# Kernel optimization log

Hardware: AMD Instinct MI355X
Metric: run time of the kernel (lower is better)

## Reference

```python
import jax, jax.numpy as jnp
import numpy as np

H = 8  # num_heads in nn.MultiheadAttention


def setup_inputs() -> dict:
    key = jax.random.key(0)
    ks = jax.random.split(key, 8)
    B, S, D, M = 32, 64, 512, 8192
    query = jax.random.normal(ks[0], (B, S, D), dtype=jnp.float32)
    memory = jax.random.normal(ks[1], (B, S, D), dtype=jnp.float32)
    memory_bank = jax.random.normal(ks[2], (M, D), dtype=jnp.float32)
    # nn.MultiheadAttention params: packed in_proj (3D, D) + bias, out_proj (D, D) + bias
    in_proj_w = jax.random.normal(ks[3], (3 * D, D), dtype=jnp.float32) / np.sqrt(D)
    in_proj_b = jnp.zeros((3 * D,), dtype=jnp.float32)
    out_proj_w = jax.random.normal(ks[4], (D, D), dtype=jnp.float32) / np.sqrt(D)
    out_proj_b = jnp.zeros((D,), dtype=jnp.float32)
    return {
        "query": query,
        "memory": memory,
        "memory_bank": memory_bank,
        "in_proj_w": in_proj_w,
        "in_proj_b": in_proj_b,
        "out_proj_w": out_proj_w,
        "out_proj_b": out_proj_b,
        "ptr": 17,
    }


def _retrieve(query, memory_bank, in_proj_w, in_proj_b, out_proj_w, out_proj_b):
    B, S, D = query.shape
    M = memory_bank.shape[0]
    hd = D // H
    Wq, Wk, Wv = in_proj_w[:D], in_proj_w[D:2 * D], in_proj_w[2 * D:]
    bq, bk, bv = in_proj_b[:D], in_proj_b[D:2 * D], in_proj_b[2 * D:]
    # key/value come from memory_bank expanded over batch -> identical per batch,
    # so project once: [M, D]
    q = (query @ Wq.T + bq).reshape(B, S, H, hd)
    k = (memory_bank @ Wk.T + bk).reshape(M, H, hd)
    v = (memory_bank @ Wv.T + bv).reshape(M, H, hd)
    scale = 1.0 / np.sqrt(hd).astype(np.float32)
    scores = jnp.einsum('bshd,mhd->bhsm', q * scale, k)  # [B,H,S,M]
    attn = jax.nn.softmax(scores, axis=-1)
    out = jnp.einsum('bhsm,mhd->bshd', attn, v).reshape(B, S, D)
    return out @ out_proj_w.T + out_proj_b


def _store(memory, memory_bank, ptr):
    M, D = memory_bank.shape
    flat = memory.reshape(-1, D)  # [N, D], N < M so indices are unique
    N = flat.shape[0]
    idx = (ptr + jnp.arange(N)) % M  # vectorized circular-buffer scatter
    new_bank = memory_bank.at[idx].set(flat)
    new_ptr = (ptr + N) % M
    return new_bank, new_ptr


def reference(query, memory, memory_bank, in_proj_w, in_proj_b, out_proj_w, out_proj_b, ptr):
    retrieved = _retrieve(query, memory_bank, in_proj_w, in_proj_b, out_proj_w, out_proj_b)
    new_bank, _ = _store(memory, memory_bank, ptr)
    return retrieved, new_bank
```

## Files before the change

### kernel.cpp

```cpp
#include <hip/hip_runtime.h>


#define Dm  512
#define Mb  8192
#define BSr 2048

#define QSCALE 0.18033688011112042f

typedef float f32x4 __attribute__((ext_vector_type(4)));
typedef short bf16x4 __attribute__((ext_vector_type(4)));
typedef short bf16x8 __attribute__((ext_vector_type(8)));
typedef unsigned short u16x4 __attribute__((ext_vector_type(4)));
typedef unsigned short u16x8 __attribute__((ext_vector_type(8)));
typedef unsigned u32x4 __attribute__((ext_vector_type(4)));

#define MFMA(a, b, c) __builtin_amdgcn_mfma_f32_16x16x32_bf16((a), (b), (c), 0, 0, 0)

#if __has_builtin(__builtin_amdgcn_exp2f)
#define EXP2F(x) __builtin_amdgcn_exp2f(x)
#else
#define EXP2F(x) __expf((x)*0.6931471805599453f)
#endif

__device__ __forceinline__ unsigned short f32_bf16(float f) {
  unsigned u = __builtin_bit_cast(unsigned, f);
  u += 0x7FFFu + ((u >> 16) & 1u);
  return (unsigned short)(u >> 16);
}
__device__ __forceinline__ float bf16_f32(unsigned short h) {
  unsigned u = ((unsigned)h) << 16;
  return __builtin_bit_cast(float, u);
}
__device__ __forceinline__ unsigned pack_bf16_trunc(float a, float b) {
  return (__builtin_bit_cast(unsigned, a) >> 16) |
         (__builtin_bit_cast(unsigned, b) & 0xFFFF0000u);
}

__device__ __forceinline__ void gload16(const unsigned short* g, unsigned short* l) {
  __builtin_amdgcn_global_load_lds(
      (const __attribute__((address_space(1))) void*)g,
      (__attribute__((address_space(3))) void*)l, 16, 0, 0);
}

__global__ __launch_bounds__(256) void convert_all(
    const float* __restrict__ q, const float* __restrict__ bank,
    const float* __restrict__ Win, const float* __restrict__ bin,
    const float* __restrict__ Wout, const float* __restrict__ bout,
    unsigned short* __restrict__ q_c, unsigned short* __restrict__ bank_c,
    unsigned short* __restrict__ Win_c, unsigned short* __restrict__ bin_c,
    unsigned short* __restrict__ Wout_c, unsigned short* __restrict__ bout_c) {
  const int e = (blockIdx.x * 256 + threadIdx.x) * 4;
  const float* src; unsigned short* dst; int off; int sw;
  if (e < 1048576)      { src = q;    dst = q_c;    off = e;           sw = 1; }
  else if (e < 5242880) { src = bank; dst = bank_c; off = e - 1048576; sw = 1; }
  else if (e < 6029312) { src = Win;  dst = Win_c;  off = e - 5242880; sw = 1; }
  else if (e < 6030848) { src = bin;  dst = bin_c;  off = e - 6029312; sw = 0; }
  else if (e < 6292992) { src = Wout; dst = Wout_c; off = e - 6030848; sw = 1; }
  else                  { src = bout; dst = bout_c; off = e - 6292992; sw = 0; }
  f32x4 v = *(const f32x4*)(src + off);
  u16x4 o;
#pragma unroll
  for (int j = 0; j < 4; ++j) o[j] = f32_bf16(v[j]);
  int doff = off;
  if (sw) {
    const int row = off >> 9, col = off & 511;
    doff = (off & ~511) | ((((col >> 3) ^ (row & 7)) << 3) | (col & 7));
  }
  *(u16x4*)(dst + doff) = o;
}

__global__ __launch_bounds__(256, 2) void proj_fused(
    const unsigned short* __restrict__ q_c,
    const unsigned short* __restrict__ bank_c,
    const unsigned short* __restrict__ Win_c,
    const unsigned short* __restrict__ bin_c,
    unsigned short* __restrict__ q_s,
    unsigned short* __restrict__ k_s,
    unsigned short* __restrict__ vT_s) {
  __shared__ __align__(16) unsigned short sh[32768];
  const int lane = threadIdx.x & 63;
  const int wv   = threadIdx.x >> 6;
  const int l15  = lane & 15;
  const int qd   = lane >> 4;
  const int mh   = wv & 1;
  const int nh   = wv >> 1;

  const unsigned short *Ag, *B0, *B1;
  int h = 0, mbase, nbase = 0;
  const bool iskv = blockIdx.x < 512;
  if (iskv) {
    const int idx = blockIdx.x;
    h     = (idx >> 3) & 7;
    mbase = ((idx & 7) * 8 + (idx >> 6)) * 128;
    Ag = bank_c + mbase * Dm;
    B0 = Win_c + (Dm + h * 64) * Dm;
    B1 = Win_c + (2 * Dm + h * 64) * Dm;
  } else {
    const int idx = blockIdx.x - 512;
    mbase = (idx >> 2) * 128;
    nbase = (idx & 3) * 128;
    Ag = q_c + mbase * Dm;
    B0 = Win_c + nbase * Dm;
    B1 = Win_c + (nbase + 64) * Dm;
  }

  auto Ab = [&](int buf) { return sh + buf * 8192; };
  auto Bb = [&](int buf) { return sh + 16384 + buf * 8192; };

  auto stage = [&](int buf, int t) {
#pragma unroll
    for (int i = 0; i < 4; ++i) {
      const int chunk = i * 256 + wv * 64 + lane;
      const int row = chunk >> 3, c8 = chunk & 7;
      gload16(Ag + row * Dm + (t * 8 + c8) * 8,
              Ab(buf) + (i * 256 + wv * 64) * 8);
    }
#pragma unroll
    for (int i = 0; i < 4; ++i) {
      const int chunk = i * 256 + wv * 64 + lane;
      const int row = chunk >> 3, c8 = chunk & 7;
      const unsigned short* wb = (row < 64) ? B0 + row * Dm : B1 + (row - 64) * Dm;
      gload16(wb + (t * 8 + c8) * 8,
              Bb(buf) + (i * 256 + wv * 64) * 8);
    }
  };

  const f32x4 z4 = {0.f, 0.f, 0.f, 0.f};
  f32x4 acc[4][4];
#pragma unroll
  for (int mt = 0; mt < 4; ++mt)
#pragma unroll
    for (int nt = 0; nt < 4; ++nt) acc[mt][nt] = z4;

  auto compute = [&](int buf) {
#pragma unroll
    for (int ks = 0; ks < 2; ++ks) {
      bf16x8 af[4], bfr[4];
#pragma unroll
      for (int mt = 0; mt < 4; ++mt) {
        const int row = mh * 64 + mt * 16 + l15;
        af[mt] = *(const bf16x8*)(Ab(buf) + row * 64 + (((ks * 4 + qd) ^ (row & 7)) * 8));
      }
#pragma unroll
      for (int nt = 0; nt < 4; ++nt) {
        const int row = nh * 64 + nt * 16 + l15;
        bfr[nt] = *(const bf16x8*)(Bb(buf) + row * 64 + (((ks * 4 + qd) ^ (row & 7)) * 8));
      }
#pragma unroll
      for (int mt = 0; mt < 4; ++mt)
#pragma unroll
        for (int nt = 0; nt < 4; ++nt)
          acc[mt][nt] = MFMA(af[mt], bfr[nt], acc[mt][nt]);
    }
  };

  stage(0, 0);
  __asm__ volatile("s_waitcnt vmcnt(0)" ::: "memory");
  __syncthreads();
#pragma unroll 1
  for (int t = 0; t < 7; ++t) {
    stage((t + 1) & 1, t + 1);
    compute(t & 1);
    __asm__ volatile("s_waitcnt vmcnt(0)" ::: "memory");
    __syncthreads();
  }
  compute(1);
  __syncthreads();

  if (iskv) {
    unsigned short* Kst = sh;
    unsigned short* Vst = sh + 16384;
    if (nh == 0) {
#pragma unroll
      for (int nt = 0; nt < 4; ++nt) {
        const int d = nt * 16 + l15;
        const float bk = bf16_f32(bin_c[Dm + h * 64 + d]);
#pragma unroll
        for (int mt = 0; mt < 4; ++mt)
#pragma unroll
          for (int r = 0; r < 4; ++r) {
            const int m = mh * 64 + mt * 16 + qd * 4 + r;
            Kst[m * 72 + d] = f32_bf16(acc[mt][nt][r] + bk);
          }
      }
    } else {
#pragma unroll
      for (int nt = 0; nt < 4; ++nt) {
        const int d = nt * 16 + l15;
        const float bv = bf16_f32(bin_c[2 * Dm + h * 64 + d]);
#pragma unroll
        for (int mt = 0; mt < 4; ++mt)
#pragma unroll
          for (int r = 0; r < 4; ++r) {
            const int m = mh * 64 + mt * 16 + qd * 4 + r;
            Vst[d * 136 + m] = f32_bf16(acc[mt][nt][r] + bv);
          }
      }
    }
    __syncthreads();
#pragma unroll
    for (int p = 0; p < 4; ++p) {
      const int m  = p * 32 + (threadIdx.x >> 3);
      const int c8 = threadIdx.x & 7;
      *(u16x8*)(k_s + h * (Mb * 64) + (mbase + m) * 64 + ((c8 ^ (m & 7)) * 8)) =
          *(const u16x8*)(Kst + m * 72 + c8 * 8);
    }
#pragma unroll
    for (int p = 0; p < 4; ++p) {
      const int d    = p * 16 + (threadIdx.x >> 4);
      const int m16  = threadIdx.x & 15;
      const int base = (m16 >> 2) * 32;
      const int q4   = (m16 & 3) * 4;
      u16x4 lo = *(const u16x4*)(Vst + d * 136 + base + q4);
      u16x4 hi = *(const u16x4*)(Vst + d * 136 + base + 16 + q4);
      u16x8 o  = __builtin_shufflevector(lo, hi, 0, 1, 2, 3, 4, 5, 6, 7);
      *(u16x8*)(vT_s + (h * 64 + d) * Mb + mbase + ((m16 ^ (d & 7)) * 8)) = o;
    }
  } else {
#pragma unroll
    for (int nt = 0; nt < 4; ++nt) {
      const int n = nbase + nh * 64 + nt * 16 + l15;
      const float bf = bf16_f32(bin_c[n]);
#pragma unroll
      for (int mt = 0; mt < 4; ++mt)
#pragma unroll
        for (int r = 0; r < 4; ++r) {
          const int m = mbase + mh * 64 + mt * 16 + qd * 4 + r;
          const unsigned idx = ((unsigned)(m >> 6) * 8u + (unsigned)(n >> 6)) * 4096u +
                               (unsigned)(m & 63) * 64u + (unsigned)(n & 63);
          q_s[idx] = f32_bf16((acc[mt][nt][r] + bf) * QSCALE);
        }
    }
  }
}

__global__ __launch_bounds__(256, 2) void attn_partial(
    const unsigned short* __restrict__ q_s,
    const unsigned short* __restrict__ k_s,
    const unsigned short* __restrict__ vT_s,
    unsigned short* __restrict__ O_part,
    float* __restrict__ l_part) {
  __shared__ __align__(16) unsigned short Kbuf[2][128 * 64];
  __shared__ __align__(16) unsigned short Vbuf[2][64 * 128];

  const int lane = threadIdx.x & 63;
  const int wv   = threadIdx.x >> 6;
  const int l15  = lane & 15;
  const int qd   = lane >> 4;
  const int h    = blockIdx.x & 7;
  const int g    = blockIdx.x >> 3;
  const int part = g & 3;
  const int b    = (g >> 2) * 2 + (wv >> 1);
  const int bh   = b * 8 + h;
  const int s0   = (wv & 1) * 32;

  const unsigned short* kp = k_s  + h * (Mb * 64);
  const unsigned short* vp = vT_s + h * (Mb * 64);
  const int m0p = part * 2048;

  bf16x8 bQ[2][2];
  {
    const unsigned short* qp = q_s + bh * 4096;
#pragma unroll
    for (int sj = 0; sj < 2; ++sj)
#pragma unroll
      for (int ks = 0; ks < 2; ++ks)
        bQ[sj][ks] = *(const bf16x8*)(qp + (s0 + sj * 16 + l15) * 64 + ks * 32 + qd * 8);
  }

  const f32x4 z4 = {0.f, 0.f, 0.f, 0.f};
  f32x4 oacc[2][4];
  float lsum[2] = {0.f, 0.f};
#pragma unroll
  for (int sj = 0; sj < 2; ++sj)
#pragma unroll
    for (int dt = 0; dt < 4; ++dt) oacc[sj][dt] = z4;

  const int swz = (l15 & 7) * 8;

  auto stage = [&](int buf, int m0) {
    const unsigned short* gk = kp + (m0 + wv * 32 + (lane >> 3)) * 64 + (lane & 7) * 8;
    unsigned short* lk = &Kbuf[buf][(wv * 32) * 64];
#pragma unroll
    for (int i = 0; i < 4; ++i) gload16(gk + i * 8 * 64, lk + i * 8 * 64);
    const unsigned short* gv = vp + (wv * 16 + (lane >> 4)) * Mb + m0 + (lane & 15) * 8;
    unsigned short* lv = &Vbuf[buf][(wv * 16) * 128];
#pragma unroll
    for (int i = 0; i < 4; ++i) gload16(gv + i * 4 * Mb, lv + i * 4 * 128);
  };

  auto compute = [&](int buf) {
    const unsigned short* Kb = Kbuf[buf];
    const unsigned short* Vb = Vbuf[buf];
#pragma unroll
    for (int c2 = 0; c2 < 2; ++c2) {
      f32x4 sfr[4][2];
#pragma unroll
      for (int kt = 0; kt < 4; ++kt)
#pragma unroll
        for (int sj = 0; sj < 2; ++sj) sfr[kt][sj] = z4;
#pragma unroll
      for (int kt = 0; kt < 4; ++kt) {
        const int row = c2 * 64 + kt * 16 + l15;
#pragma unroll
        for (int ks = 0; ks < 2; ++ks) {
          bf16x8 aK = *(const bf16x8*)(Kb + row * 64 + ((ks * 32 + qd * 8) ^ swz));
#pragma unroll
          for (int sj = 0; sj < 2; ++sj)
            sfr[kt][sj] = MFMA(aK, bQ[sj][ks], sfr[kt][sj]);
        }
      }
      bf16x8 aP[2][2];
#pragma unroll
      for (int sj = 0; sj < 2; ++sj) {
#pragma unroll
        for (int c = 0; c < 2; ++c) {
          const f32x4 lo = sfr[c * 2][sj];
          const f32x4 hi = sfr[c * 2 + 1][sj];
          float e0 = EXP2F(lo[0]), e1 = EXP2F(lo[1]);
          float e2 = EXP2F(lo[2]), e3 = EXP2F(lo[3]);
          float e4 = EXP2F(hi[0]), e5 = EXP2F(hi[1]);
          float e6 = EXP2F(hi[2]), e7 = EXP2F(hi[3]);
          lsum[sj] += ((e0 + e1) + (e2 + e3)) + ((e4 + e5) + (e6 + e7));
          u32x4 pk;
          pk[0] = pack_bf16_trunc(e0, e1);
          pk[1] = pack_bf16_trunc(e2, e3);
          pk[2] = pack_bf16_trunc(e4, e5);
          pk[3] = pack_bf16_trunc(e6, e7);
          aP[sj][c] = __builtin_bit_cast(bf16x8, pk);
        }
      }
#pragma unroll
      for (int c = 0; c < 2; ++c) {
#pragma unroll
        for (int dt = 0; dt < 4; ++dt) {
          const int d = dt * 16 + l15;
          bf16x8 bV = *(const bf16x8*)(Vb + d * 128 + ((c2 * 64 + c * 32 + qd * 8) ^ swz));
#pragma unroll
          for (int sj = 0; sj < 2; ++sj)
            oacc[sj][dt] = MFMA(aP[sj][c], bV, oacc[sj][dt]);
        }
      }
    }
  };

  stage(0, m0p);
  __asm__ volatile("s_waitcnt vmcnt(0)" ::: "memory");
  __syncthreads();
#pragma unroll 1
  for (int t = 0; t < 15; ++t) {
    stage((t + 1) & 1, m0p + (t + 1) * 128);
    compute(t & 1);
    __asm__ volatile("s_waitcnt vmcnt(0)" ::: "memory");
    __syncthreads();
  }
  compute(1);

#pragma unroll
  for (int sj = 0; sj < 2; ++sj) {
    float v = lsum[sj];
    v += __shfl_xor(v, 16);
    v += __shfl_xor(v, 32);
    if (qd == 0) l_part[(bh * 4 + part) * 64 + s0 + sj * 16 + l15] = v;
  }

  unsigned short* Ob = O_part + (bh * 4 + part) * 4096;
#pragma unroll
  for (int sj = 0; sj < 2; ++sj)
#pragma unroll
    for (int dt = 0; dt < 4; ++dt)
#pragma unroll
      for (int r = 0; r < 4; ++r)
        Ob[(s0 + sj * 16 + qd * 4 + r) * 64 + dt * 16 + l15] = f32_bf16(oacc[sj][dt][r]);
}

__global__ __launch_bounds__(256) void combine_bank(
    const unsigned short* __restrict__ O_part, const float* __restrict__ l_part,
    unsigned short* __restrict__ a_stage,
    const float* __restrict__ memory, const float* __restrict__ bank,
    const int* __restrict__ ptrp, float* __restrict__ out_bank) {
  if (blockIdx.x < 1024) {
    const int e  = (blockIdx.x * 256 + threadIdx.x) * 4;
    const int bh = e >> 12;
    const int rem = e & 4095;
    const int s  = rem >> 6;
    const int d  = rem & 63;
    float acc[4] = {0.f, 0.f, 0.f, 0.f};
    float l = 0.f;
#pragma unroll
    for (int p = 0; p < 4; ++p) {
      u16x4 v = *(const u16x4*)(O_part + (bh * 4 + p) * 4096 + rem);
#pragma unroll
      for (int j = 0; j < 4; ++j) acc[j] += bf16_f32(v[j]);
      l += l_part[(bh * 4 + p) * 64 + s];
    }
    const int b = bh >> 3, h = bh & 7;
    u16x4 o;
#pragma unroll
    for (int j = 0; j < 4; ++j) o[j] = f32_bf16(acc[j] / l);
    const int row = b * 64 + s;
    const int col = h * 64 + d;
    const int scol = (((col >> 3) ^ (row & 7)) << 3) | (col & 7);
    *(u16x4*)(a_stage + row * 512 + scol) = o;
  } else {
    const int t  = (blockIdx.x - 1024) * 256 + threadIdx.x;
    const int r  = t >> 7;
    const int c4 = (t & 127) * 4;
    const int ptr = ptrp[0];
    const unsigned off = (unsigned)(r - ptr + Mb) & (Mb - 1);
    const float* src = (off < (unsigned)BSr) ? memory + off * Dm + c4
                                             : bank + r * Dm + c4;
    *(f32x4*)(out_bank + r * Dm + c4) = *(const f32x4*)src;
  }
}

__global__ __launch_bounds__(256, 2) void out_proj(
    const unsigned short* __restrict__ A,
    const unsigned short* __restrict__ W,
    const unsigned short* __restrict__ bias,
    float* __restrict__ out) {
  __shared__ __align__(16) unsigned short sh[32768];
  const int lane = threadIdx.x & 63;
  const int wv   = threadIdx.x >> 6;
  const int l15  = lane & 15;
  const int qd   = lane >> 4;
  const int mh   = wv & 1;
  const int nh   = wv >> 1;

  const int mbase = (blockIdx.x >> 2) * 128;
  const int nbase = (blockIdx.x & 3) * 128;
  const unsigned short* Ag = A + mbase * Dm;
  const unsigned short* B0 = W + nbase * Dm;
  const unsigned short* B1 = W + (nbase + 64) * Dm;

  auto Ab = [&](int buf) { return sh + buf * 8192; };
  auto Bb = [&](int buf) { return sh + 16384 + buf * 8192; };

  auto stage = [&](int buf, int t) {
#pragma unroll
    for (int i = 0; i < 4; ++i) {
      const int chunk = i * 256 + wv * 64 + lane;
      const int row = chunk >> 3, c8 = chunk & 7;
      gload16(Ag + row * Dm + (t * 8 + c8) * 8,
              Ab(buf) + (i * 256 + wv * 64) * 8);
    }
#pragma unroll
    for (int i = 0; i < 4; ++i) {
      const int chunk = i * 256 + wv * 64 + lane;
      const int row = chunk >> 3, c8 = chunk & 7;
      const unsigned short* wb = (row < 64) ? B0 + row * Dm : B1 + (row - 64) * Dm;
      gload16(wb + (t * 8 + c8) * 8,
              Bb(buf) + (i * 256 + wv * 64) * 8);
    }
  };

  const f32x4 z4 = {0.f, 0.f, 0.f, 0.f};
  f32x4 acc[4][4];
#pragma unroll
  for (int mt = 0; mt < 4; ++mt)
#pragma unroll
    for (int nt = 0; nt < 4; ++nt) acc[mt][nt] = z4;

  auto compute = [&](int buf) {
#pragma unroll
    for (int ks = 0; ks < 2; ++ks) {
      bf16x8 af[4], bfr[4];
#pragma unroll
      for (int mt = 0; mt < 4; ++mt) {
        const int row = mh * 64 + mt * 16 + l15;
        af[mt] = *(const bf16x8*)(Ab(buf) + row * 64 + (((ks * 4 + qd) ^ (row & 7)) * 8));
      }
#pragma unroll
      for (int nt = 0; nt < 4; ++nt) {
        const int row = nh * 64 + nt * 16 + l15;
        bfr[nt] = *(const bf16x8*)(Bb(buf) + row * 64 + (((ks * 4 + qd) ^ (row & 7)) * 8));
      }
#pragma unroll
      for (int mt = 0; mt < 4; ++mt)
#pragma unroll
        for (int nt = 0; nt < 4; ++nt)
          acc[mt][nt] = MFMA(af[mt], bfr[nt], acc[mt][nt]);
    }
  };

  stage(0, 0);
  __asm__ volatile("s_waitcnt vmcnt(0)" ::: "memory");
  __syncthreads();
#pragma unroll 1
  for (int t = 0; t < 7; ++t) {
    stage((t + 1) & 1, t + 1);
    compute(t & 1);
    __asm__ volatile("s_waitcnt vmcnt(0)" ::: "memory");
    __syncthreads();
  }
  compute(1);

#pragma unroll
  for (int nt = 0; nt < 4; ++nt) {
    const int n = nbase + nh * 64 + nt * 16 + l15;
    const float bf = bf16_f32(bias[n]);
#pragma unroll
    for (int mt = 0; mt < 4; ++mt)
#pragma unroll
      for (int r = 0; r < 4; ++r) {
        const int m = mbase + mh * 64 + mt * 16 + qd * 4 + r;
        out[m * Dm + n] = acc[mt][nt][r] + bf;
      }
  }
}

extern "C" void kernel_launch(void* const* d_in, const int* in_sizes, int n_in,
                              void* d_out, int out_size, void* d_ws, size_t ws_size,
                              hipStream_t stream) {
  const float* query = (const float*)d_in[0];
  const float* memry = (const float*)d_in[1];
  const float* bank  = (const float*)d_in[2];
  const float* Win   = (const float*)d_in[3];
  const float* bin   = (const float*)d_in[4];
  const float* Wout  = (const float*)d_in[5];
  const float* bout  = (const float*)d_in[6];
  const int*   ptrp  = (const int*)d_in[7];
  float* outf = (float*)d_out;

  char* ws = (char*)d_ws;
  unsigned short* q_c     = (unsigned short*)(ws);
  unsigned short* a_stage = (unsigned short*)(ws);
  unsigned short* bank_c  = (unsigned short*)(ws + (2u << 20));
  unsigned short* O_part  = (unsigned short*)(ws + (2u << 20));
  unsigned short* Win_c   = (unsigned short*)(ws + (10u << 20));
  unsigned short* Wout_c  = (unsigned short*)(ws + 12058624u);
  unsigned short* q_s     = (unsigned short*)(ws + (12u << 20));
  float*          l_part  = (float*)(ws + (14u << 20));
  unsigned short* bin_c   = (unsigned short*)(ws + 14942208u);
  unsigned short* bout_c  = (unsigned short*)(ws + 14945280u);

  unsigned short* kv = (unsigned short*)(outf + 1048576);
  unsigned short* k_s  = kv;
  unsigned short* vT_s = kv + 4194304;

  convert_all<<<6146, 256, 0, stream>>>(query, bank, Win, bin, Wout, bout,
                                        q_c, bank_c, Win_c, bin_c, Wout_c, bout_c);

  proj_fused<<<576, 256, 0, stream>>>(q_c, bank_c, Win_c, bin_c, q_s, k_s, vT_s);

  attn_partial<<<512, 256, 0, stream>>>(q_s, k_s, vT_s, O_part, l_part);

  combine_bank<<<5120, 256, 0, stream>>>(O_part, l_part, a_stage,
                                         memry, bank, ptrp, outf + 1048576);

  out_proj<<<64, 256, 0, stream>>>(a_stage, Wout_c, bout_c, outf);
}
```

Baseline: 160.0 us.

## Split attention key tiles across wave pairs with LDS reduction of partial outputs

```diff
diff --git a/kernel.cpp b/kernel.cpp
--- a/kernel.cpp
+++ b/kernel.cpp
@@ -234,14 +234,14 @@
   }
 }
 
-__global__ __launch_bounds__(256, 2) void attn_partial(
+__global__ __launch_bounds__(512, 4) void attn_partial(
     const unsigned short* __restrict__ q_s,
     const unsigned short* __restrict__ k_s,
     const unsigned short* __restrict__ vT_s,
     unsigned short* __restrict__ O_part,
     float* __restrict__ l_part) {
-  __shared__ __align__(16) unsigned short Kbuf[2][128 * 64];
-  __shared__ __align__(16) unsigned short Vbuf[2][64 * 128];
+  __shared__ __align__(16) unsigned short shmem[2][2][64 * 64];
+  __shared__ float lred[256];
 
   const int lane = threadIdx.x & 63;
   const int wv   = threadIdx.x >> 6;
@@ -250,9 +250,11 @@
   const int h    = blockIdx.x & 7;
   const int g    = blockIdx.x >> 3;
   const int part = g & 3;
-  const int b    = (g >> 2) * 2 + (wv >> 1);
-  const int bh   = b * 8 + h;
-  const int s0   = (wv & 1) * 32;
+  const int bp   = g >> 2;
+  const int bsel = wv >> 2;
+  const int sh_  = (wv >> 1) & 1;
+  const int kh   = (wv & 1) * 32;
+  const int bh   = (bp * 2 + bsel) * 8 + h;
 
   const unsigned short* kp = k_s  + h * (Mb * 64);
   const unsigned short* vp = vT_s + h * (Mb * 64);
@@ -265,7 +267,8 @@
     for (int sj = 0; sj < 2; ++sj)
 #pragma unroll
       for (int ks = 0; ks < 2; ++ks)
-        bQ[sj][ks] = *(const bf16x8*)(qp + (s0 + sj * 16 + l15) * 64 + ks * 32 + qd * 8);
+        bQ[sj][ks] = *(const bf16x8*)(qp + (sh_ * 32 + sj * 16 + l15) * 64 +
+                                      ks * 32 + qd * 8);
   }
 
   const f32x4 z4 = {0.f, 0.f, 0.f, 0.f};
@@ -279,68 +282,51 @@
   const int swz = (l15 & 7) * 8;
 
   auto stage = [&](int buf, int m0) {
-    const unsigned short* gk = kp + (m0 + wv * 32 + (lane >> 3)) * 64 + (lane & 7) * 8;
-    unsigned short* lk = &Kbuf[buf][(wv * 32) * 64];
-#pragma unroll
-    for (int i = 0; i < 4; ++i) gload16(gk + i * 8 * 64, lk + i * 8 * 64);
-    const unsigned short* gv = vp + (wv * 16 + (lane >> 4)) * Mb + m0 + (lane & 15) * 8;
-    unsigned short* lv = &Vbuf[buf][(wv * 16) * 128];
-#pragma unroll
-    for (int i = 0; i < 4; ++i) gload16(gv + i * 4 * Mb, lv + i * 4 * 128);
+    const int r8 = lane >> 3, c8 = lane & 7;
+    gload16(kp + (m0 + wv * 8 + r8) * 64 + c8 * 8, &shmem[buf][0][(wv * 8) * 64]);
+    gload16(vp + (wv * 8 + r8) * Mb + m0 + c8 * 8, &shmem[buf][1][(wv * 8) * 64]);
   };
 
   auto compute = [&](int buf) {
-    const unsigned short* Kb = Kbuf[buf];
-    const unsigned short* Vb = Vbuf[buf];
-#pragma unroll
-    for (int c2 = 0; c2 < 2; ++c2) {
-      f32x4 sfr[4][2];
-#pragma unroll
-      for (int kt = 0; kt < 4; ++kt)
-#pragma unroll
-        for (int sj = 0; sj < 2; ++sj) sfr[kt][sj] = z4;
-#pragma unroll
-      for (int kt = 0; kt < 4; ++kt) {
-        const int row = c2 * 64 + kt * 16 + l15;
-#pragma unroll
-        for (int ks = 0; ks < 2; ++ks) {
-          bf16x8 aK = *(const bf16x8*)(Kb + row * 64 + ((ks * 32 + qd * 8) ^ swz));
-#pragma unroll
-          for (int sj = 0; sj < 2; ++sj)
-            sfr[kt][sj] = MFMA(aK, bQ[sj][ks], sfr[kt][sj]);
-        }
-      }
-      bf16x8 aP[2][2];
-#pragma unroll
-      for (int sj = 0; sj < 2; ++sj) {
-#pragma unroll
-        for (int c = 0; c < 2; ++c) {
-          const f32x4 lo = sfr[c * 2][sj];
-          const f32x4 hi = sfr[c * 2 + 1][sj];
-          float e0 = EXP2F(lo[0]), e1 = EXP2F(lo[1]);
-          float e2 = EXP2F(lo[2]), e3 = EXP2F(lo[3]);
-          float e4 = EXP2F(hi[0]), e5 = EXP2F(hi[1]);
-          float e6 = EXP2F(hi[2]), e7 = EXP2F(hi[3]);
-          lsum[sj] += ((e0 + e1) + (e2 + e3)) + ((e4 + e5) + (e6 + e7));
-          u32x4 pk;
-          pk[0] = pack_bf16_trunc(e0, e1);
-          pk[1] = pack_bf16_trunc(e2, e3);
-          pk[2] = pack_bf16_trunc(e4, e5);
-          pk[3] = pack_bf16_trunc(e6, e7);
-          aP[sj][c] = __builtin_bit_cast(bf16x8, pk);
-        }
-      }
-#pragma unroll
-      for (int c = 0; c < 2; ++c) {
-#pragma unroll
-        for (int dt = 0; dt < 4; ++dt) {
-          const int d = dt * 16 + l15;
-          bf16x8 bV = *(const bf16x8*)(Vb + d * 128 + ((c2 * 64 + c * 32 + qd * 8) ^ swz));
-#pragma unroll
-          for (int sj = 0; sj < 2; ++sj)
-            oacc[sj][dt] = MFMA(aP[sj][c], bV, oacc[sj][dt]);
-        }
-      }
+    const unsigned short* Kb = &shmem[buf][0][0];
+    const unsigned short* Vb = &shmem[buf][1][0];
+    f32x4 sfr[2][2];
+#pragma unroll
+    for (int kt = 0; kt < 2; ++kt)
+#pragma unroll
+      for (int sj = 0; sj < 2; ++sj) sfr[kt][sj] = z4;
+#pragma unroll
+    for (int kt = 0; kt < 2; ++kt) {
+      const int row = kh + kt * 16 + l15;
+#pragma unroll
+      for (int ks = 0; ks < 2; ++ks) {
+        bf16x8 aK = *(const bf16x8*)(Kb + row * 64 + ((ks * 32 + qd * 8) ^ swz));
+#pragma unroll
+        for (int sj = 0; sj < 2; ++sj)
+          sfr[kt][sj] = MFMA(aK, bQ[sj][ks], sfr[kt][sj]);
+      }
+    }
+    bf16x8 aP[2];
+#pragma unroll
+    for (int sj = 0; sj < 2; ++sj) {
+      float e0 = EXP2F(sfr[0][sj][0]), e1 = EXP2F(sfr[0][sj][1]);
+      float e2 = EXP2F(sfr[0][sj][2]), e3 = EXP2F(sfr[0][sj][3]);
+      float e4 = EXP2F(sfr[1][sj][0]), e5 = EXP2F(sfr[1][sj][1]);
+      float e6 = EXP2F(sfr[1][sj][2]), e7 = EXP2F(sfr[1][sj][3]);
+      lsum[sj] += ((e0 + e1) + (e2 + e3)) + ((e4 + e5) + (e6 + e7));
+      u32x4 pk;
+      pk[0] = pack_bf16_trunc(e0, e1);
+      pk[1] = pack_bf16_trunc(e2, e3);
+      pk[2] = pack_bf16_trunc(e4, e5);
+      pk[3] = pack_bf16_trunc(e6, e7);
+      aP[sj] = __builtin_bit_cast(bf16x8, pk);
+    }
+#pragma unroll
+    for (int dt = 0; dt < 4; ++dt) {
+      bf16x8 bV = *(const bf16x8*)(Vb + (dt * 16 + l15) * 64 + ((kh + qd * 8) ^ swz));
+#pragma unroll
+      for (int sj = 0; sj < 2; ++sj)
+        oacc[sj][dt] = MFMA(aP[sj], bV, oacc[sj][dt]);
     }
   };
 
@@ -348,8 +334,8 @@
   __asm__ volatile("s_waitcnt vmcnt(0)" ::: "memory");
   __syncthreads();
 #pragma unroll 1
-  for (int t = 0; t < 15; ++t) {
-    stage((t + 1) & 1, m0p + (t + 1) * 128);
+  for (int t = 0; t < 31; ++t) {
+    stage((t + 1) & 1, m0p + (t + 1) * 64);
     compute(t & 1);
     __asm__ volatile("s_waitcnt vmcnt(0)" ::: "memory");
     __syncthreads();
@@ -361,17 +347,49 @@
     float v = lsum[sj];
     v += __shfl_xor(v, 16);
     v += __shfl_xor(v, 32);
-    if (qd == 0) l_part[(bh * 4 + part) * 64 + s0 + sj * 16 + l15] = v;
-  }
-
-  unsigned short* Ob = O_part + (bh * 4 + part) * 4096;
-#pragma unroll
-  for (int sj = 0; sj < 2; ++sj)
-#pragma unroll
-    for (int dt = 0; dt < 4; ++dt)
-#pragma unroll
-      for (int r = 0; r < 4; ++r)
-        Ob[(s0 + sj * 16 + qd * 4 + r) * 64 + dt * 16 + l15] = f32_bf16(oacc[sj][dt][r]);
+    if (qd == 0) lred[wv * 32 + sj * 16 + l15] = v;
+  }
+  __syncthreads();
+
+  if (threadIdx.x < 128) {
+    const int bs = threadIdx.x >> 6, s = threadIdx.x & 63;
+    const int bh2 = (bp * 2 + bs) * 8 + h;
+    const int w0 = bs * 4 + (s >> 5) * 2;
+    l_part[(bh2 * 4 + part) * 64 + s] =
+        lred[w0 * 32 + (s & 31)] + lred[(w0 + 1) * 32 + (s & 31)];
+  }
+
+  float* red = (float*)&shmem[0][0][0];
+#pragma unroll 1
+  for (int bs = 0; bs < 2; ++bs) {
+    if (bsel == bs) {
+      const int w4 = (wv & 3);
+#pragma unroll
+      for (int sj = 0; sj < 2; ++sj)
+#pragma unroll
+        for (int dt = 0; dt < 4; ++dt)
+#pragma unroll
+          for (int r = 0; r < 4; ++r)
+            red[(((w4 * 2 + sj) * 4 + dt) * 4 + r) * 64 + lane] = oacc[sj][dt][r];
+    }
+    __syncthreads();
+    const int bh2 = (bp * 2 + bs) * 8 + h;
+    unsigned short* Ob = O_part + (bh2 * 4 + part) * 4096;
+#pragma unroll
+    for (int i = 0; i < 8; ++i) {
+      const int idx  = i * 512 + threadIdx.x;
+      const int srow = idx >> 6, dcol = idx & 63;
+      const int sh2 = srow >> 5, sj = (srow >> 4) & 1;
+      const int qq  = (srow >> 2) & 3, r = srow & 3;
+      const int dt  = dcol >> 4, ll = dcol & 15;
+      const int ln  = qq * 16 + ll;
+      const float v =
+          red[((((sh2 * 2 + 0) * 2 + sj) * 4 + dt) * 4 + r) * 64 + ln] +
+          red[((((sh2 * 2 + 1) * 2 + sj) * 4 + dt) * 4 + r) * 64 + ln];
+      Ob[srow * 64 + dcol] = f32_bf16(v);
+    }
+    __syncthreads();
+  }
 }
 
 __global__ __launch_bounds__(256) void combine_bank(
@@ -543,7 +561,7 @@
 
   proj_fused<<<576, 256, 0, stream>>>(q_c, bank_c, Win_c, bin_c, q_s, k_s, vT_s);
 
-  attn_partial<<<512, 256, 0, stream>>>(q_s, k_s, vT_s, O_part, l_part);
+  attn_partial<<<512, 512, 0, stream>>>(q_s, k_s, vT_s, O_part, l_part);
 
   combine_bank<<<5120, 256, 0, stream>>>(O_part, l_part, a_stage,
                                          memry, bank, ptrp, outf + 1048576);
```

Measured after the change: 166.6 us. +4.1%, slower.
